# Kernel tuning notes

Hardware: AMD Instinct MI355X
Metric: run time of the kernel (lower is better)

The kernel has to match this reference:

```python
import jax, jax.numpy as jnp
import numpy as np

IN_C, OUT_C, K, STRIDE, PAD = 64, 128, 3, 1, 1


def setup_inputs() -> dict:
    key = jax.random.key(0)
    kx, kw = jax.random.split(key)
    x = jax.random.normal(kx, (16, IN_C, 112, 112), dtype=jnp.float32)
    scale = np.sqrt(2.0 / (IN_C * K * K)).astype(np.float32)
    weight = jax.random.normal(kw, (OUT_C, IN_C, K, K), dtype=jnp.float32) * scale
    bias = jnp.zeros((OUT_C,), dtype=jnp.float32)
    return {"x": x, "weight": weight, "bias": bias}


def reference(x, weight, bias):
    # Direct 2D convolution (cross-correlation, like torch Conv2d), NCHW layout.
    out = jax.lax.conv_general_dilated(
        x, weight,
        window_strides=(STRIDE, STRIDE),
        padding=((PAD, PAD), (PAD, PAD)),
        dimension_numbers=("NCHW", "OIHW", "NCHW"),
    )
    return out + bias[None, :, None, None]
```

## Files before the change

### kernel.cpp

```cpp
#include <hip/hip_runtime.h>
#include <stdint.h>


#define HW     112
#define PIX    12544
#define ICN    64
#define OCN    128
#define TILEP  128
#define PTILES 98
#define NBLK   1568
#define NIMG   16

#define XT_BYTES   (NIMG * PIX * ICN * 2)
#define WT_OFF     XT_BYTES
#define WT_BYTES   (9 * OCN * ICN * 2)
#define ZG_OFF     (WT_OFF + WT_BYTES)
#define XBLK       (NIMG * (PIX / 64))
#define WBLK       72

typedef __attribute__((ext_vector_type(8))) __bf16 bf16x8;
typedef __attribute__((ext_vector_type(4))) float  f32x4;

__device__ __forceinline__ uint32_t rne_lo(float f) {
    uint32_t u = __builtin_bit_cast(uint32_t, f);
    return (u + 0x7fffu + ((u >> 16) & 1u)) >> 16;
}
__device__ __forceinline__ uint32_t pk2(float a, float b) {
    uint32_t ub = __builtin_bit_cast(uint32_t, b);
    ub = (ub + 0x7fffu + ((ub >> 16) & 1u)) & 0xffff0000u;
    return rne_lo(a) | ub;
}

__device__ __forceinline__ void load_lds16(const void* g, void* l) {
    __builtin_amdgcn_global_load_lds(
        (const __attribute__((address_space(1))) uint32_t*)g,
        (__attribute__((address_space(3))) uint32_t*)l, 16, 0, 0);
}

__global__ void __launch_bounds__(256)
prep(const float* __restrict__ x, const float* __restrict__ w, uint8_t* __restrict__ ws) {
    const int b = blockIdx.x;
    const int t = threadIdx.x;
    uint16_t* xt = (uint16_t*)ws;
    uint16_t* wt = (uint16_t*)(ws + WT_OFF);

    if (b < XBLK) {
        const int n  = b / (PIX / 64);
        const int p0 = (b - n * (PIX / 64)) * 64;
        const int px = t >> 2;
        const int q  = t & 3;
        const float* src = x + ((size_t)n * ICN + q * 16) * PIX + p0 + px;
        float v[16];
#pragma unroll
        for (int i = 0; i < 16; ++i) v[i] = src[(size_t)i * PIX];
        uint4 u0 = make_uint4(pk2(v[0], v[1]),  pk2(v[2], v[3]),
                              pk2(v[4], v[5]),  pk2(v[6], v[7]));
        uint4 u1 = make_uint4(pk2(v[8], v[9]),  pk2(v[10], v[11]),
                              pk2(v[12], v[13]), pk2(v[14], v[15]));
        char* dst = (char*)xt + ((size_t)(n * PIX + p0 + px)) * 128 + q * 32;
        *(uint4*)dst        = u0;
        *(uint4*)(dst + 16) = u1;
    } else {
        const int wb = b - XBLK;
#pragma unroll
        for (int k = 0; k < 4; ++k) {
            int wi = wb * 1024 + k * 256 + t;
            int r  = wi >> 13;
            int oc = (wi >> 6) & 127;
            int ic = wi & 63;
            wt[wi] = (uint16_t)rne_lo(w[oc * 576 + ic * 9 + r]);
        }
        if (wb == 0 && t < 8) ((uint4*)(ws + ZG_OFF))[t] = make_uint4(0, 0, 0, 0);
    }
}

__global__ void __launch_bounds__(256)
conv_mfma(const uint8_t* __restrict__ ws, const float* __restrict__ bias,
          float* __restrict__ out) {
    __shared__ uint16_t As[8192];
    __shared__ uint16_t Xs[8192];

    const char* xt = (const char*)ws;
    const char* wt = (const char*)(ws + WT_OFF);
    const char* zg = (const char*)(ws + ZG_OFF);

    const int t = threadIdx.x;
    const int b = blockIdx.x;
    const int n_img = b / PTILES;
    const int p0 = (b - n_img * PTILES) * TILEP;

    const int lane = t & 63;
    const int wave = t >> 6;
    const int lr = lane & 15;
    const int lq = lane >> 4;
    const int oc_base = (wave & 1) * 64;
    const int px_base = (wave >> 1) * 64;

    const int rowB = t >> 3;
    const int cswz = (t & 7) ^ (rowB & 7);
    int sh[4], sw[4];
    const char* xaddr[4];
#pragma unroll
    for (int r2 = 0; r2 < 4; ++r2) {
        int row = r2 * 32 + rowB;
        int p = p0 + row;
        int hh = p / HW;
        sh[r2] = hh;
        sw[r2] = p - hh * HW;
        xaddr[r2] = xt + ((size_t)(n_img * PIX + p)) * 128 + cswz * 16;
    }
    const char* waddr0 = wt + rowB * 128 + cswz * 16;
    const char* zaddr  = zg + (t & 7) * 16;

    f32x4 acc[4][4];
    {
        f32x4 z = {0.f, 0.f, 0.f, 0.f};
#pragma unroll
        for (int i = 0; i < 4; ++i)
#pragma unroll
            for (int j = 0; j < 4; ++j) acc[i][j] = z;
    }

#pragma unroll
    for (int tap = 0; tap < 9; ++tap) {
        const int dy = tap / 3 - 1;
        const int dx = tap - (tap / 3) * 3 - 1;
        const int toff = (dy * HW + dx) * 128;

        __syncthreads();

#pragma unroll
        for (int r2 = 0; r2 < 4; ++r2)
            load_lds16(waddr0 + tap * 16384 + r2 * 4096,
                       (char*)As + r2 * 4096 + wave * 1024);
#pragma unroll
        for (int r2 = 0; r2 < 4; ++r2) {
            int hh = sh[r2] + dy;
            int wwp = sw[r2] + dx;
            bool ok = ((unsigned)hh < HW) & ((unsigned)wwp < HW);
            const char* gp = ok ? (xaddr[r2] + toff) : zaddr;
            load_lds16(gp, (char*)Xs + r2 * 4096 + wave * 1024);
        }

        __syncthreads();

#pragma unroll
        for (int kh = 0; kh < 2; ++kh) {
            bf16x8 a_frag[4], b_frag[4];
            const int cc = kh * 4 + lq;
#pragma unroll
            for (int mi = 0; mi < 4; ++mi) {
                int R = oc_base + mi * 16 + lr;
                a_frag[mi] = *(const bf16x8*)((const char*)As + R * 128 + ((cc ^ (R & 7)) * 16));
            }
#pragma unroll
            for (int ni = 0; ni < 4; ++ni) {
                int R = px_base + ni * 16 + lr;
                b_frag[ni] = *(const bf16x8*)((const char*)Xs + R * 128 + ((cc ^ (R & 7)) * 16));
            }
#pragma unroll
            for (int mi = 0; mi < 4; ++mi)
#pragma unroll
                for (int ni = 0; ni < 4; ++ni)
                    acc[mi][ni] = __builtin_amdgcn_mfma_f32_16x16x32_bf16(
                        a_frag[mi], b_frag[ni], acc[mi][ni], 0, 0, 0);
        }
    }

#pragma unroll
    for (int mi = 0; mi < 4; ++mi) {
#pragma unroll
        for (int rg = 0; rg < 4; ++rg) {
            const int oc = oc_base + mi * 16 + lq * 4 + rg;
            const float bb = bias[oc];
            float* orow = out + ((size_t)n_img * OCN + oc) * PIX + p0 + px_base + lr;
#pragma unroll
            for (int ni = 0; ni < 4; ++ni)
                orow[ni * 16] = acc[mi][ni][rg] + bb;
        }
    }
}

extern "C" void kernel_launch(void* const* d_in, const int* in_sizes, int n_in,
                              void* d_out, int out_size, void* d_ws, size_t ws_size,
                              hipStream_t stream) {
    const float* x    = (const float*)d_in[0];
    const float* w    = (const float*)d_in[1];
    const float* bias = (const float*)d_in[2];
    float* out = (float*)d_out;
    uint8_t* ws = (uint8_t*)d_ws;

    prep<<<XBLK + WBLK, 256, 0, stream>>>(x, w, ws);
    conv_mfma<<<NBLK, 256, 0, stream>>>(ws, bias, out);
}
```

Baseline: 174.4 us.

## Zero-pad input in prep and reuse one halo row tile across all taps

The prep kernel now writes a zero-padded 114x114 NHWC bf16 image, which removes per-tap bounds checks and the zero-page trick. Each conv block covers two output rows: it loads the 4-row padded halo into LDS once and reuses it for all 9 taps, so the per-tap syncthreads and global-to-LDS reloads go away. Weights are read directly from global memory (L2/L1) into registers rather than staged through LDS. This lowers redundant input traffic and barrier cost, but raises register pressure (28 accumulator tiles plus 8 A fragments) and leaves fewer blocks (896), which may hurt occupancy and load balance.

```diff
diff --git a/kernel.cpp b/kernel.cpp
--- a/kernel.cpp
+++ b/kernel.cpp
@@ -2,21 +2,20 @@
 #include <stdint.h>
 
 
-#define HW     112
-#define PIX    12544
-#define ICN    64
-#define OCN    128
-#define TILEP  128
-#define PTILES 98
-#define NBLK   1568
-#define NIMG   16
+#define HW      112
+#define PIX     12544
+#define ICN     64
+#define OCN     128
+#define PADW    114
+#define PADPIX  12996
+#define NIMG    16
 
-#define XT_BYTES   (NIMG * PIX * ICN * 2)
-#define WT_OFF     XT_BYTES
-#define WT_BYTES   (9 * OCN * ICN * 2)
-#define ZG_OFF     (WT_OFF + WT_BYTES)
-#define XBLK       (NIMG * (PIX / 64))
-#define WBLK       72
+#define XT_BYTES  (NIMG * PADPIX * ICN * 2)
+#define WT_OFF    XT_BYTES
+#define XPB       204
+#define XBLK      (NIMG * XPB)
+#define WBLK      72
+#define CONV_BLK  (NIMG * 56)
 
 typedef __attribute__((ext_vector_type(8))) __bf16 bf16x8;
 typedef __attribute__((ext_vector_type(4))) float  f32x4;
@@ -30,7 +29,6 @@
     ub = (ub + 0x7fffu + ((ub >> 16) & 1u)) & 0xffff0000u;
     return rne_lo(a) | ub;
 }
-
 __device__ __forceinline__ void load_lds16(const void* g, void* l) {
     __builtin_amdgcn_global_load_lds(
         (const __attribute__((address_space(1))) uint32_t*)g,
@@ -41,26 +39,31 @@
 prep(const float* __restrict__ x, const float* __restrict__ w, uint8_t* __restrict__ ws) {
     const int b = blockIdx.x;
     const int t = threadIdx.x;
-    uint16_t* xt = (uint16_t*)ws;
-    uint16_t* wt = (uint16_t*)(ws + WT_OFF);
 
     if (b < XBLK) {
-        const int n  = b / (PIX / 64);
-        const int p0 = (b - n * (PIX / 64)) * 64;
-        const int px = t >> 2;
+        const int n  = b / XPB;
+        const int pp = (b - n * XPB) * 64 + (t >> 2);
         const int q  = t & 3;
-        const float* src = x + ((size_t)n * ICN + q * 16) * PIX + p0 + px;
-        float v[16];
+        if (pp >= PADPIX) return;
+        char* dst = (char*)ws + ((size_t)(n * PADPIX + pp)) * 128 + q * 32;
+        const int hp = pp / PADW;
+        const int wp = pp - hp * PADW;
+        if (hp >= 1 && hp <= HW && wp >= 1 && wp <= HW) {
+            const int p = (hp - 1) * HW + (wp - 1);
+            const float* src = x + ((size_t)n * ICN + q * 16) * PIX + p;
+            float v[16];
 #pragma unroll
-        for (int i = 0; i < 16; ++i) v[i] = src[(size_t)i * PIX];
-        uint4 u0 = make_uint4(pk2(v[0], v[1]),  pk2(v[2], v[3]),
-                              pk2(v[4], v[5]),  pk2(v[6], v[7]));
-        uint4 u1 = make_uint4(pk2(v[8], v[9]),  pk2(v[10], v[11]),
-                              pk2(v[12], v[13]), pk2(v[14], v[15]));
-        char* dst = (char*)xt + ((size_t)(n * PIX + p0 + px)) * 128 + q * 32;
-        *(uint4*)dst        = u0;
-        *(uint4*)(dst + 16) = u1;
+            for (int i = 0; i < 16; ++i) v[i] = src[(size_t)i * PIX];
+            *(uint4*)dst        = make_uint4(pk2(v[0], v[1]),   pk2(v[2], v[3]),
+                                             pk2(v[4], v[5]),   pk2(v[6], v[7]));
+            *(uint4*)(dst + 16) = make_uint4(pk2(v[8], v[9]),   pk2(v[10], v[11]),
+                                             pk2(v[12], v[13]), pk2(v[14], v[15]));
+        } else {
+            *(uint4*)dst        = make_uint4(0, 0, 0, 0);
+            *(uint4*)(dst + 16) = make_uint4(0, 0, 0, 0);
+        }
     } else {
+        uint16_t* wt = (uint16_t*)(ws + WT_OFF);
         const int wb = b - XBLK;
 #pragma unroll
         for (int k = 0; k < 4; ++k) {
@@ -70,112 +73,98 @@
             int ic = wi & 63;
             wt[wi] = (uint16_t)rne_lo(w[oc * 576 + ic * 9 + r]);
         }
-        if (wb == 0 && t < 8) ((uint4*)(ws + ZG_OFF))[t] = make_uint4(0, 0, 0, 0);
     }
 }
 
-__global__ void __launch_bounds__(256)
+__global__ void __launch_bounds__(256, 2)
 conv_mfma(const uint8_t* __restrict__ ws, const float* __restrict__ bias,
           float* __restrict__ out) {
-    __shared__ uint16_t As[8192];
-    __shared__ uint16_t Xs[8192];
+    __shared__ uint8_t Xs[4 * PADW * 128];
 
     const char* xt = (const char*)ws;
     const char* wt = (const char*)(ws + WT_OFF);
-    const char* zg = (const char*)(ws + ZG_OFF);
 
     const int t = threadIdx.x;
     const int b = blockIdx.x;
-    const int n_img = b / PTILES;
-    const int p0 = (b - n_img * PTILES) * TILEP;
+    const int n  = b / 56;
+    const int tr = b - n * 56;
+    const int h0 = tr * 2;
 
     const int lane = t & 63;
     const int wave = t >> 6;
     const int lr = lane & 15;
     const int lq = lane >> 4;
     const int oc_base = (wave & 1) * 64;
-    const int px_base = (wave >> 1) * 64;
+    const int pxb = wave >> 1;
 
-    const int rowB = t >> 3;
-    const int cswz = (t & 7) ^ (rowB & 7);
-    int sh[4], sw[4];
-    const char* xaddr[4];
+    {
+        const char* hbase = xt + ((size_t)(n * PADPIX + h0 * PADW)) * 128;
 #pragma unroll
-    for (int r2 = 0; r2 < 4; ++r2) {
-        int row = r2 * 32 + rowB;
-        int p = p0 + row;
-        int hh = p / HW;
-        sh[r2] = hh;
-        sw[r2] = p - hh * HW;
-        xaddr[r2] = xt + ((size_t)(n_img * PIX + p)) * 128 + cswz * 16;
+        for (int i = 0; i < 14; ++i) {
+            const int idx = i * 256 + t;
+            const int r = idx >> 3, c = idx & 7;
+            load_lds16(hbase + r * 128 + ((c ^ (r & 7)) * 16),
+                       (char*)Xs + (i * 256 + wave * 64) * 16);
+        }
+        if (wave == 0) {
+            const int idx = 14 * 256 + t;
+            const int r = idx >> 3, c = idx & 7;
+            load_lds16(hbase + r * 128 + ((c ^ (r & 7)) * 16),
+                       (char*)Xs + (14 * 256) * 16);
+        }
     }
-    const char* waddr0 = wt + rowB * 128 + cswz * 16;
-    const char* zaddr  = zg + (t & 7) * 16;
+    __syncthreads();
 
-    f32x4 acc[4][4];
+    f32x4 acc[4][7];
     {
         f32x4 z = {0.f, 0.f, 0.f, 0.f};
 #pragma unroll
         for (int i = 0; i < 4; ++i)
 #pragma unroll
-            for (int j = 0; j < 4; ++j) acc[i][j] = z;
+            for (int j = 0; j < 7; ++j) acc[i][j] = z;
     }
+
+    const char* abase = wt + (oc_base + lr) * 128 + lq * 16;
 
 #pragma unroll
     for (int tap = 0; tap < 9; ++tap) {
         const int dy = tap / 3 - 1;
         const int dx = tap - (tap / 3) * 3 - 1;
-        const int toff = (dy * HW + dx) * 128;
+        const int rb = (pxb + dy + 1) * PADW + dx + 1 + lr;
+        const int s0 = ((lq)     ^ (rb & 7)) * 16;
+        const int s1 = ((lq + 4) ^ (rb & 7)) * 16;
+        const char* bbase = (const char*)Xs + rb * 128;
 
-        __syncthreads();
-
+        bf16x8 a[8];
 #pragma unroll
-        for (int r2 = 0; r2 < 4; ++r2)
-            load_lds16(waddr0 + tap * 16384 + r2 * 4096,
-                       (char*)As + r2 * 4096 + wave * 1024);
+        for (int mi = 0; mi < 4; ++mi) {
+            a[mi * 2]     = *(const bf16x8*)(abase + tap * 16384 + mi * 2048);
+            a[mi * 2 + 1] = *(const bf16x8*)(abase + tap * 16384 + mi * 2048 + 64);
+        }
 #pragma unroll
-        for (int r2 = 0; r2 < 4; ++r2) {
-            int hh = sh[r2] + dy;
-            int wwp = sw[r2] + dx;
-            bool ok = ((unsigned)hh < HW) & ((unsigned)wwp < HW);
-            const char* gp = ok ? (xaddr[r2] + toff) : zaddr;
-            load_lds16(gp, (char*)Xs + r2 * 4096 + wave * 1024);
-        }
-
-        __syncthreads();
-
-#pragma unroll
-        for (int kh = 0; kh < 2; ++kh) {
-            bf16x8 a_frag[4], b_frag[4];
-            const int cc = kh * 4 + lq;
+        for (int ni = 0; ni < 7; ++ni) {
+            bf16x8 b0 = *(const bf16x8*)(bbase + ni * 2048 + s0);
+            bf16x8 b1 = *(const bf16x8*)(bbase + ni * 2048 + s1);
 #pragma unroll
             for (int mi = 0; mi < 4; ++mi) {
-                int R = oc_base + mi * 16 + lr;
-                a_frag[mi] = *(const bf16x8*)((const char*)As + R * 128 + ((cc ^ (R & 7)) * 16));
+                acc[mi][ni] = __builtin_amdgcn_mfma_f32_16x16x32_bf16(
+                    a[mi * 2],     b0, acc[mi][ni], 0, 0, 0);
+                acc[mi][ni] = __builtin_amdgcn_mfma_f32_16x16x32_bf16(
+                    a[mi * 2 + 1], b1, acc[mi][ni], 0, 0, 0);
             }
-#pragma unroll
-            for (int ni = 0; ni < 4; ++ni) {
-                int R = px_base + ni * 16 + lr;
-                b_frag[ni] = *(const bf16x8*)((const char*)Xs + R * 128 + ((cc ^ (R & 7)) * 16));
-            }
-#pragma unroll
-            for (int mi = 0; mi < 4; ++mi)
-#pragma unroll
-                for (int ni = 0; ni < 4; ++ni)
-                    acc[mi][ni] = __builtin_amdgcn_mfma_f32_16x16x32_bf16(
-                        a_frag[mi], b_frag[ni], acc[mi][ni], 0, 0, 0);
         }
     }
 
+    const int oh = h0 + pxb;
 #pragma unroll
     for (int mi = 0; mi < 4; ++mi) {
 #pragma unroll
         for (int rg = 0; rg < 4; ++rg) {
             const int oc = oc_base + mi * 16 + lq * 4 + rg;
             const float bb = bias[oc];
-            float* orow = out + ((size_t)n_img * OCN + oc) * PIX + p0 + px_base + lr;
+            float* orow = out + ((size_t)(n * OCN + oc)) * PIX + oh * HW + lr;
 #pragma unroll
-            for (int ni = 0; ni < 4; ++ni)
+            for (int ni = 0; ni < 7; ++ni)
                 orow[ni * 16] = acc[mi][ni][rg] + bb;
         }
     }
@@ -191,5 +180,5 @@
     uint8_t* ws = (uint8_t*)d_ws;
 
     prep<<<XBLK + WBLK, 256, 0, stream>>>(x, w, ws);
-    conv_mfma<<<NBLK, 256, 0, stream>>>(ws, bias, out);
+    conv_mfma<<<CONV_BLK, 256, 0, stream>>>(ws, bias, out);
 }
```

Result: slower. 187.6 us (+7.6%).
